# Kernel optimization log

Measured on AMD Instinct MI355X. Metric: run time of the kernel, lower is better.

Reference implementation:

```python
import jax, jax.numpy as jnp
import numpy as np

B, N, M, D, H = 4, 384, 384, 64, 64


def _lin(key, fi, fo):
    kw, kb = jax.random.split(key)
    bound = 1.0 / np.sqrt(fi)
    W = jax.random.uniform(kw, (fi, fo), jnp.float32, -bound, bound)
    b = jax.random.uniform(kb, (fo,), jnp.float32, -bound, bound)
    return W, b


def setup_inputs() -> dict:
    key = jax.random.key(0)
    kX, kY, kp = jax.random.split(key, 3)
    X = jax.random.normal(kX, (B, N, D), jnp.float32)
    Y = jax.random.normal(kY, (B, M, D), jnp.float32)
    ks = jax.random.split(kp, 10)
    inp = {"X": X, "Y": Y}
    # Four pair encoders (e1_xx, e1_xy, e1_yx, e1_yy): Linear(2D,H) -> ReLU -> Linear(H,H)
    for i, tag in enumerate(["xx", "xy", "yx", "yy"]):
        W1, b1 = _lin(ks[2 * i], 2 * D, H)
        W2, b2 = _lin(ks[2 * i + 1], H, H)
        inp[f"W_{tag}1"], inp[f"b_{tag}1"] = W1, b1
        inp[f"W_{tag}2"], inp[f"b_{tag}2"] = W2, b2
    # Decoder: Linear(2H,H) -> ReLU -> Linear(H,1)
    inp["Wd1"], inp["bd1"] = _lin(ks[8], 2 * H, H)
    inp["Wd2"], inp["bd2"] = _lin(ks[9], H, 1)
    return inp


def _pair_branch(A, C, W1, b1, W2, b2):
    """Encode pairs cat(A[b,j], C[b,i]) with MLP, then max over j.

    Instead of materializing the [B,I,J,2D] concat tensor, split the first
    linear layer: cat(a, c) @ W1 == a @ W1[:D] + c @ W1[D:].
    Returns [B, I, H].
    """
    Da = A.shape[-1]
    pa = jnp.einsum('bjd,dh->bjh', A, W1[:Da])   # contribution of A[b, j]
    pc = jnp.einsum('bid,dh->bih', C, W1[Da:])   # contribution of C[b, i]
    pre = pa[:, None, :, :] + pc[:, :, None, :] + b1          # [B, I, J, H]
    h = jnp.einsum('bijh,hk->bijk', jax.nn.relu(pre), W2) + b2  # [B, I, J, H]
    return jnp.max(h, axis=2)                                   # [B, I, H]


def reference(X, Y,
              W_xx1, b_xx1, W_xx2, b_xx2,
              W_xy1, b_xy1, W_xy2, b_xy2,
              W_yx1, b_yx1, W_yx2, b_yx2,
              W_yy1, b_yy1, W_yy2, b_yy2,
              Wd1, bd1, Wd2, bd2):
    # XX[b,i,j] = cat(X[b,j], X[b,i]); YX[b,i,j] = cat(Y[b,j], X[b,i]); etc.
    Z_XX = _pair_branch(X, X, W_xx1, b_xx1, W_xx2, b_xx2)  # [B, N, H]
    Z_YX = _pair_branch(Y, X, W_yx1, b_yx1, W_yx2, b_yx2)  # [B, N, H]
    # Computed in the original forward but never used downstream (dead code):
    Z_YY = _pair_branch(Y, Y, W_yy1, b_yy1, W_yy2, b_yy2)  # noqa: F841
    Z_XY = _pair_branch(X, Y, W_xy1, b_xy1, W_xy2, b_xy2)  # noqa: F841
    # Original source sets Z_Y = Z_XX - Z_YX as well (apparent bug, preserved).
    diff = Z_XX - Z_YX
    Z_X = jnp.sum(diff, axis=1)  # [B, H]
    Z_Y = jnp.sum(diff, axis=1)  # [B, H]
    z = jnp.concatenate([Z_X, Z_Y], axis=-1)        # [B, 2H]
    h = jax.nn.relu(z @ Wd1 + bd1)
    return h @ Wd2 + bd2                             # [B, 1]
```

## Files before the change

### kernel.cpp

```cpp
#include <hip/hip_runtime.h>

#define B_ 4
#define N_ 384
#define D_ 64
#define H_ 64
#define BN_ (B_ * N_)
#define ROW_ (N_ * H_)
#define NTP_ 12
#define LDW_ 68

typedef float f32x4 __attribute__((ext_vector_type(4)));
typedef _Float16 half8 __attribute__((ext_vector_type(8)));
typedef __fp16 fp16x2 __attribute__((ext_vector_type(2)));

union frag_cast { f32x4 f; half8 h; };

__global__ __launch_bounds__(256) void proj_kernel(
    const float* __restrict__ X, const float* __restrict__ Y,
    const float* __restrict__ Wxx1, const float* __restrict__ bxx1,
    const float* __restrict__ Wyx1, const float* __restrict__ byx1,
    const float* __restrict__ W2xx, const float* __restrict__ W2yx,
    float* __restrict__ PAxx, float* __restrict__ PCxx,
    float* __restrict__ PAyx, float* __restrict__ PCyx,
    _Float16* __restrict__ W2F)
{
    if (blockIdx.x >= 384) {
        int t = (blockIdx.x - 384) * 256 + threadIdx.x;
        int br = t >> 10;
        int q  = (t >> 6) & 15;
        int l  = t & 63;
        int nt = q >> 2, kt = (q >> 1) & 1, part = q & 1;
        const float* W2 = br ? W2yx : W2xx;
        int n = nt * 16 + (l & 15);
        int g = l >> 4;
        _Float16* dst = W2F + t * 8;
#pragma unroll
        for (int e = 0; e < 8; ++e) {
            int h = kt * 32 + g * 8 + e;
            float v = W2[h * 64 + n];
            _Float16 hi = (_Float16)v;
            _Float16 lo = (_Float16)(v - (float)hi);
            dst[e] = part ? lo : hi;
        }
        return;
    }

    int blk = blockIdx.x;
    int t = threadIdx.x;
    int which = t >> 6, h = t & 63;

    __shared__ float xr[4][64];
    __shared__ float yr[4][64];
    xr[t >> 6][t & 63] = X[(blk * 4 + (t >> 6)) * 64 + (t & 63)];
    yr[t >> 6][t & 63] = Y[(blk * 4 + (t >> 6)) * 64 + (t & 63)];
    __syncthreads();

    const float (*v)[64] = (which == 2) ? yr : xr;
    const float* W = (which < 2) ? Wxx1 : Wyx1;
    int rowoff = (which & 1) ? 64 : 0;

    float acc[4];
    float binit = 0.f;
    if (which == 1) binit = bxx1[h];
    if (which == 3) binit = byx1[h];
#pragma unroll
    for (int r = 0; r < 4; ++r) acc[r] = binit;

#pragma unroll
    for (int d = 0; d < 64; ++d) {
        float wv = W[(rowoff + d) * 64 + h];
#pragma unroll
        for (int r = 0; r < 4; ++r)
            acc[r] = fmaf(v[r][d], wv, acc[r]);
    }

    float* dst = (which == 0) ? PAxx : (which == 1) ? PCxx
               : (which == 2) ? PAyx : PCyx;
#pragma unroll
    for (int r = 0; r < 4; ++r)
        dst[(blk * 4 + r) * 64 + h] = acc[r];
}

__global__ __launch_bounds__(256, 3) void pair_mfma_kernel(
    const float* __restrict__ PAxx, const float* __restrict__ PCxx,
    const float* __restrict__ PAyx, const float* __restrict__ PCyx,
    const f32x4* __restrict__ W2F,
    float* __restrict__ zxxs, float* __restrict__ zyxs)
{
    int bid = blockIdx.x;
    int blk = (bid & 7) * 96 + (bid >> 3);
    int br = blk / 384;
    int ig = blk % 384;
    int t = threadIdx.x;
    int w = t >> 6, l = t & 63;
    int g = l >> 4, m = l & 15;
    int bi = ig * 4 + w;
    int b  = bi / N_;

    const float* PA = br ? PAyx : PAxx;
    const float* PC = br ? PCyx : PCxx;

    __shared__ float lbuf[2][32 * LDW_];
    __shared__ float zsums[4][64];

    half8 bf[4][2][2];
    const f32x4* Wb = W2F + br * 1024;
#pragma unroll
    for (int q = 0; q < 16; ++q) {
        frag_cast u;
        u.f = Wb[q * 64 + l];
        asm volatile("" : "+v"(u.f));
        bf[q >> 2][(q >> 1) & 1][q & 1] = u.h;
    }

    f32x4 pcq[4];
#pragma unroll
    for (int kt = 0; kt < 2; ++kt) {
        pcq[kt * 2 + 0] = *(const f32x4*)(PC + bi * 64 + kt * 32 + g * 8);
        pcq[kt * 2 + 1] = *(const f32x4*)(PC + bi * 64 + kt * 32 + g * 8 + 4);
    }

    float mm[4] = {-3.0e38f, -3.0e38f, -3.0e38f, -3.0e38f};

    int srow = t >> 4;
    int scg  = t & 15;
    const float* gsrc = PA + b * ROW_ + srow * 64 + scg * 4;
    int soff = srow * LDW_ + scg * 4;

    *(f32x4*)(&lbuf[0][0] + soff) = *(const f32x4*)(gsrc);
    *(f32x4*)(&lbuf[0][0] + soff + 16 * LDW_) = *(const f32x4*)(gsrc + 1024);
    __syncthreads();

    const f32x4 vzero = {0.f, 0.f, 0.f, 0.f};
    int cur = 0;

#pragma unroll 1
    for (int pt = 0; pt < NTP_; ++pt) {
        f32x4 gn0, gn1;
        if (pt + 1 < NTP_) {
            gn0 = *(const f32x4*)(gsrc + (pt + 1) * 2048);
            gn1 = *(const f32x4*)(gsrc + (pt + 1) * 2048 + 1024);
        }

#pragma unroll
        for (int st = 0; st < 2; ++st) {
            const float* lrd = &lbuf[0][0] + cur * (32 * LDW_)
                             + (st * 16 + m) * LDW_ + g * 8;
            f32x4 s0 = *(const f32x4*)(lrd);
            f32x4 s1 = *(const f32x4*)(lrd + 4);
            f32x4 s2 = *(const f32x4*)(lrd + 32);
            f32x4 s3 = *(const f32x4*)(lrd + 36);

            half8 ah[2], al[2];
#pragma unroll
            for (int kt = 0; kt < 2; ++kt) {
                f32x4 xa = (kt ? s2 : s0) + pcq[kt * 2 + 0];
                f32x4 xb = (kt ? s3 : s1) + pcq[kt * 2 + 1];
                xa = __builtin_elementwise_max(xa, vzero);
                xb = __builtin_elementwise_max(xb, vzero);
                fp16x2* ahp = (fp16x2*)&ah[kt];
                fp16x2* alp = (fp16x2*)&al[kt];
#pragma unroll
                for (int p2 = 0; p2 < 2; ++p2) {
                    fp16x2 hpa = __builtin_amdgcn_cvt_pkrtz(xa[p2 * 2], xa[p2 * 2 + 1]);
                    fp16x2 hpb = __builtin_amdgcn_cvt_pkrtz(xb[p2 * 2], xb[p2 * 2 + 1]);
                    ahp[p2]     = hpa;
                    ahp[p2 + 2] = hpb;
                    alp[p2]     = __builtin_amdgcn_cvt_pkrtz(xa[p2 * 2]     - (float)hpa[0],
                                                             xa[p2 * 2 + 1] - (float)hpa[1]);
                    alp[p2 + 2] = __builtin_amdgcn_cvt_pkrtz(xb[p2 * 2]     - (float)hpb[0],
                                                             xb[p2 * 2 + 1] - (float)hpb[1]);
                }
            }

#pragma unroll
            for (int nt = 0; nt < 4; ++nt) {
                f32x4 a = {0.f, 0.f, 0.f, 0.f};
#pragma unroll
                for (int kt = 0; kt < 2; ++kt) {
                    a = __builtin_amdgcn_mfma_f32_16x16x32_f16(ah[kt], bf[nt][kt][0], a, 0, 0, 0);
                    a = __builtin_amdgcn_mfma_f32_16x16x32_f16(ah[kt], bf[nt][kt][1], a, 0, 0, 0);
                    a = __builtin_amdgcn_mfma_f32_16x16x32_f16(al[kt], bf[nt][kt][0], a, 0, 0, 0);
                }
                mm[nt] = fmaxf(mm[nt],
                               fmaxf(fmaxf(a[0], a[1]), fmaxf(a[2], a[3])));
            }
        }

        if (pt + 1 < NTP_) {
            *(f32x4*)(&lbuf[0][0] + (cur ^ 1) * (32 * LDW_) + soff) = gn0;
            *(f32x4*)(&lbuf[0][0] + (cur ^ 1) * (32 * LDW_) + soff + 16 * LDW_) = gn1;
        }
        __syncthreads();
        cur ^= 1;
    }

#pragma unroll
    for (int nt = 0; nt < 4; ++nt) {
        float v = mm[nt];
        v = fmaxf(v, __shfl_xor(v, 16));
        v = fmaxf(v, __shfl_xor(v, 32));
        mm[nt] = v;
    }
    float z = (l < 32) ? ((l < 16) ? mm[0] : mm[1])
                       : ((l < 48) ? mm[2] : mm[3]);

    zsums[w][l] = z;
    __syncthreads();
    if (w == 0) {
        float s = ((zsums[0][l] + zsums[1][l]) + zsums[2][l]) + zsums[3][l];
        (br ? zyxs : zxxs)[ig * 64 + l] = s;
    }
}

__global__ __launch_bounds__(256) void head_kernel(
    const float* __restrict__ zxxs, const float* __restrict__ zyxs,
    const float* __restrict__ b2xx, const float* __restrict__ b2yx,
    const float* __restrict__ Wd1, const float* __restrict__ bd1,
    const float* __restrict__ Wd2, const float* __restrict__ bd2,
    float* __restrict__ out)
{
    int b = blockIdx.x;
    int t = threadIdx.x;
    int ig = t >> 6, h = t & 63;

    __shared__ float sbuf[4][64];
    __shared__ float zx[64];

    float s = 0.f;
    for (int q = ig; q < 96; q += 4) {
        int idx = (b * 96 + q) * 64 + h;
        s += zxxs[idx] - zyxs[idx];
    }
    sbuf[ig][h] = s;
    __syncthreads();
    if (t < 64)
        zx[t] = sbuf[0][t] + sbuf[1][t] + sbuf[2][t] + sbuf[3][t]
              + (float)N_ * (b2xx[t] - b2yx[t]);
    __syncthreads();

    if (t < 64) {
        float acc = bd1[t];
#pragma unroll
        for (int d = 0; d < 64; ++d)
            acc = fmaf(zx[d], Wd1[d * 64 + t] + Wd1[(64 + d) * 64 + t], acc);
        float h1 = fmaxf(acc, 0.f);
        float r = h1 * Wd2[t];
#pragma unroll
        for (int off = 32; off; off >>= 1) r += __shfl_down(r, off);
        if (t == 0) out[b] = r + bd2[0];
    }
}

extern "C" void kernel_launch(void* const* d_in, const int* in_sizes, int n_in,
                              void* d_out, int out_size, void* d_ws, size_t ws_size,
                              hipStream_t stream) {
    const float* X    = (const float*)d_in[0];
    const float* Y    = (const float*)d_in[1];
    const float* Wxx1 = (const float*)d_in[2];
    const float* bxx1 = (const float*)d_in[3];
    const float* W2xx = (const float*)d_in[4];
    const float* b2xx = (const float*)d_in[5];
    const float* Wyx1 = (const float*)d_in[10];
    const float* byx1 = (const float*)d_in[11];
    const float* W2yx = (const float*)d_in[12];
    const float* b2yx = (const float*)d_in[13];
    const float* Wd1  = (const float*)d_in[18];
    const float* bd1  = (const float*)d_in[19];
    const float* Wd2  = (const float*)d_in[20];
    const float* bd2  = (const float*)d_in[21];

    float* ws   = (float*)d_ws;
    float* PAxx = ws;
    float* PCxx = ws + 1 * (BN_ * H_);
    float* PAyx = ws + 2 * (BN_ * H_);
    float* PCyx = ws + 3 * (BN_ * H_);
    float* zxxs = ws + 4 * (BN_ * H_);
    float* zyxs = ws + 4 * (BN_ * H_) + 384 * 64;
    _Float16* W2F = (_Float16*)(ws + 5 * (BN_ * H_));

    proj_kernel<<<384 + 8, 256, 0, stream>>>(X, Y, Wxx1, bxx1, Wyx1, byx1,
                                             W2xx, W2yx,
                                             PAxx, PCxx, PAyx, PCyx, W2F);
    pair_mfma_kernel<<<768, 256, 0, stream>>>(PAxx, PCxx, PAyx, PCyx,
                                              (const f32x4*)W2F, zxxs, zyxs);
    head_kernel<<<B_, 256, 0, stream>>>(zxxs, zyxs, b2xx, b2yx,
                                        Wd1, bd1, Wd2, bd2, (float*)d_out);
}
```

Baseline: 47.40 us.

## Switch pair MLP matmul from 16x16x32 to 32x32x16 MFMA tiles

Changes the second-layer pair matmul to use 32x32x16 f16 MFMA instructions with 16-element accumulators, covering 32 j-rows per wave in one pass instead of two 16-row subtiles. The W2 fragment preparation in the projection kernel and the B-fragment layout are rearranged to match the new operand layout. The max reduction over j shrinks to one cross-lane shuffle. The intent is to cut instruction count, LDS reads and shuffle overhead per tile, at the cost of larger accumulator register pressure, which may hurt occupancy at three waves per SIMD.

```diff
diff --git a/kernel.cpp b/kernel.cpp
--- a/kernel.cpp
+++ b/kernel.cpp
@@ -10,6 +10,7 @@
 #define LDW_ 68
 
 typedef float f32x4 __attribute__((ext_vector_type(4)));
+typedef float f32x16 __attribute__((ext_vector_type(16)));
 typedef _Float16 half8 __attribute__((ext_vector_type(8)));
 typedef __fp16 fp16x2 __attribute__((ext_vector_type(2)));
 
@@ -29,14 +30,14 @@
         int br = t >> 10;
         int q  = (t >> 6) & 15;
         int l  = t & 63;
-        int nt = q >> 2, kt = (q >> 1) & 1, part = q & 1;
+        int hc = q >> 3, ks = (q >> 1) & 3, part = q & 1;
         const float* W2 = br ? W2yx : W2xx;
-        int n = nt * 16 + (l & 15);
-        int g = l >> 4;
+        int n  = hc * 32 + (l & 31);
+        int g2 = l >> 5;
         _Float16* dst = W2F + t * 8;
 #pragma unroll
         for (int e = 0; e < 8; ++e) {
-            int h = kt * 32 + g * 8 + e;
+            int h = ks * 16 + g2 * 8 + e;
             float v = W2[h * 64 + n];
             _Float16 hi = (_Float16)v;
             _Float16 lo = (_Float16)(v - (float)hi);
@@ -93,7 +94,7 @@
     int ig = blk % 384;
     int t = threadIdx.x;
     int w = t >> 6, l = t & 63;
-    int g = l >> 4, m = l & 15;
+    int g2 = l >> 5, m32 = l & 31;
     int bi = ig * 4 + w;
     int b  = bi / N_;
 
@@ -103,24 +104,24 @@
     __shared__ float lbuf[2][32 * LDW_];
     __shared__ float zsums[4][64];
 
-    half8 bf[4][2][2];
+    half8 bf[2][4][2];
     const f32x4* Wb = W2F + br * 1024;
 #pragma unroll
     for (int q = 0; q < 16; ++q) {
         frag_cast u;
         u.f = Wb[q * 64 + l];
         asm volatile("" : "+v"(u.f));
-        bf[q >> 2][(q >> 1) & 1][q & 1] = u.h;
-    }
-
-    f32x4 pcq[4];
-#pragma unroll
-    for (int kt = 0; kt < 2; ++kt) {
-        pcq[kt * 2 + 0] = *(const f32x4*)(PC + bi * 64 + kt * 32 + g * 8);
-        pcq[kt * 2 + 1] = *(const f32x4*)(PC + bi * 64 + kt * 32 + g * 8 + 4);
-    }
-
-    float mm[4] = {-3.0e38f, -3.0e38f, -3.0e38f, -3.0e38f};
+        bf[q >> 3][(q >> 1) & 3][q & 1] = u.h;
+    }
+
+    f32x4 pcq[8];
+#pragma unroll
+    for (int ks = 0; ks < 4; ++ks) {
+        pcq[ks * 2 + 0] = *(const f32x4*)(PC + bi * 64 + ks * 16 + g2 * 8);
+        pcq[ks * 2 + 1] = *(const f32x4*)(PC + bi * 64 + ks * 16 + g2 * 8 + 4);
+    }
+
+    float mm[2] = {-3.0e38f, -3.0e38f};
 
     int srow = t >> 4;
     int scg  = t & 15;
@@ -142,49 +143,56 @@
             gn1 = *(const f32x4*)(gsrc + (pt + 1) * 2048 + 1024);
         }
 
-#pragma unroll
-        for (int st = 0; st < 2; ++st) {
-            const float* lrd = &lbuf[0][0] + cur * (32 * LDW_)
-                             + (st * 16 + m) * LDW_ + g * 8;
-            f32x4 s0 = *(const f32x4*)(lrd);
-            f32x4 s1 = *(const f32x4*)(lrd + 4);
-            f32x4 s2 = *(const f32x4*)(lrd + 32);
-            f32x4 s3 = *(const f32x4*)(lrd + 36);
-
-            half8 ah[2], al[2];
-#pragma unroll
-            for (int kt = 0; kt < 2; ++kt) {
-                f32x4 xa = (kt ? s2 : s0) + pcq[kt * 2 + 0];
-                f32x4 xb = (kt ? s3 : s1) + pcq[kt * 2 + 1];
-                xa = __builtin_elementwise_max(xa, vzero);
-                xb = __builtin_elementwise_max(xb, vzero);
-                fp16x2* ahp = (fp16x2*)&ah[kt];
-                fp16x2* alp = (fp16x2*)&al[kt];
-#pragma unroll
-                for (int p2 = 0; p2 < 2; ++p2) {
-                    fp16x2 hpa = __builtin_amdgcn_cvt_pkrtz(xa[p2 * 2], xa[p2 * 2 + 1]);
-                    fp16x2 hpb = __builtin_amdgcn_cvt_pkrtz(xb[p2 * 2], xb[p2 * 2 + 1]);
-                    ahp[p2]     = hpa;
-                    ahp[p2 + 2] = hpb;
-                    alp[p2]     = __builtin_amdgcn_cvt_pkrtz(xa[p2 * 2]     - (float)hpa[0],
-                                                             xa[p2 * 2 + 1] - (float)hpa[1]);
-                    alp[p2 + 2] = __builtin_amdgcn_cvt_pkrtz(xb[p2 * 2]     - (float)hpb[0],
-                                                             xb[p2 * 2 + 1] - (float)hpb[1]);
-                }
+        f32x16 acc0 = {0.f,0.f,0.f,0.f,0.f,0.f,0.f,0.f,
+                       0.f,0.f,0.f,0.f,0.f,0.f,0.f,0.f};
+        f32x16 acc1 = {0.f,0.f,0.f,0.f,0.f,0.f,0.f,0.f,
+                       0.f,0.f,0.f,0.f,0.f,0.f,0.f,0.f};
+
+        const float* rowbase = &lbuf[0][0] + cur * (32 * LDW_) + m32 * LDW_;
+
+#pragma unroll
+        for (int ks = 0; ks < 4; ++ks) {
+            f32x4 s0 = *(const f32x4*)(rowbase + ks * 16 + g2 * 8);
+            f32x4 s1 = *(const f32x4*)(rowbase + ks * 16 + g2 * 8 + 4);
+
+            f32x4 xa = s0 + pcq[ks * 2 + 0];
+            f32x4 xb = s1 + pcq[ks * 2 + 1];
+            xa = __builtin_elementwise_max(xa, vzero);
+            xb = __builtin_elementwise_max(xb, vzero);
+            half8 ah, al;
+            fp16x2* ahp = (fp16x2*)&ah;
+            fp16x2* alp = (fp16x2*)&al;
+#pragma unroll
+            for (int p2 = 0; p2 < 2; ++p2) {
+                fp16x2 hpa = __builtin_amdgcn_cvt_pkrtz(xa[p2 * 2], xa[p2 * 2 + 1]);
+                fp16x2 hpb = __builtin_amdgcn_cvt_pkrtz(xb[p2 * 2], xb[p2 * 2 + 1]);
+                ahp[p2]     = hpa;
+                ahp[p2 + 2] = hpb;
+                alp[p2]     = __builtin_amdgcn_cvt_pkrtz(xa[p2 * 2]     - (float)hpa[0],
+                                                         xa[p2 * 2 + 1] - (float)hpa[1]);
+                alp[p2 + 2] = __builtin_amdgcn_cvt_pkrtz(xb[p2 * 2]     - (float)hpb[0],
+                                                         xb[p2 * 2 + 1] - (float)hpb[1]);
             }
 
-#pragma unroll
-            for (int nt = 0; nt < 4; ++nt) {
-                f32x4 a = {0.f, 0.f, 0.f, 0.f};
-#pragma unroll
-                for (int kt = 0; kt < 2; ++kt) {
-                    a = __builtin_amdgcn_mfma_f32_16x16x32_f16(ah[kt], bf[nt][kt][0], a, 0, 0, 0);
-                    a = __builtin_amdgcn_mfma_f32_16x16x32_f16(ah[kt], bf[nt][kt][1], a, 0, 0, 0);
-                    a = __builtin_amdgcn_mfma_f32_16x16x32_f16(al[kt], bf[nt][kt][0], a, 0, 0, 0);
-                }
-                mm[nt] = fmaxf(mm[nt],
-                               fmaxf(fmaxf(a[0], a[1]), fmaxf(a[2], a[3])));
-            }
+            acc0 = __builtin_amdgcn_mfma_f32_32x32x16_f16(ah, bf[0][ks][0], acc0, 0, 0, 0);
+            acc1 = __builtin_amdgcn_mfma_f32_32x32x16_f16(ah, bf[1][ks][0], acc1, 0, 0, 0);
+            acc0 = __builtin_amdgcn_mfma_f32_32x32x16_f16(al, bf[0][ks][0], acc0, 0, 0, 0);
+            acc1 = __builtin_amdgcn_mfma_f32_32x32x16_f16(al, bf[1][ks][0], acc1, 0, 0, 0);
+            acc0 = __builtin_amdgcn_mfma_f32_32x32x16_f16(ah, bf[0][ks][1], acc0, 0, 0, 0);
+            acc1 = __builtin_amdgcn_mfma_f32_32x32x16_f16(ah, bf[1][ks][1], acc1, 0, 0, 0);
+        }
+
+        {
+            float a0 = fmaxf(fmaxf(acc0[0], acc0[1]), fmaxf(acc0[2], acc0[3]));
+            float a1 = fmaxf(fmaxf(acc0[4], acc0[5]), fmaxf(acc0[6], acc0[7]));
+            float a2 = fmaxf(fmaxf(acc0[8], acc0[9]), fmaxf(acc0[10], acc0[11]));
+            float a3 = fmaxf(fmaxf(acc0[12], acc0[13]), fmaxf(acc0[14], acc0[15]));
+            mm[0] = fmaxf(mm[0], fmaxf(fmaxf(a0, a1), fmaxf(a2, a3)));
+            float c0 = fmaxf(fmaxf(acc1[0], acc1[1]), fmaxf(acc1[2], acc1[3]));
+            float c1 = fmaxf(fmaxf(acc1[4], acc1[5]), fmaxf(acc1[6], acc1[7]));
+            float c2 = fmaxf(fmaxf(acc1[8], acc1[9]), fmaxf(acc1[10], acc1[11]));
+            float c3 = fmaxf(fmaxf(acc1[12], acc1[13]), fmaxf(acc1[14], acc1[15]));
+            mm[1] = fmaxf(mm[1], fmaxf(fmaxf(c0, c1), fmaxf(c2, c3)));
         }
 
         if (pt + 1 < NTP_) {
@@ -195,15 +203,9 @@
         cur ^= 1;
     }
 
-#pragma unroll
-    for (int nt = 0; nt < 4; ++nt) {
-        float v = mm[nt];
-        v = fmaxf(v, __shfl_xor(v, 16));
-        v = fmaxf(v, __shfl_xor(v, 32));
-        mm[nt] = v;
-    }
-    float z = (l < 32) ? ((l < 16) ? mm[0] : mm[1])
-                       : ((l < 48) ? mm[2] : mm[3]);
+    float v0 = fmaxf(mm[0], __shfl_xor(mm[0], 32));
+    float v1 = fmaxf(mm[1], __shfl_xor(mm[1], 32));
+    float z = (l < 32) ? v0 : v1;
 
     zsums[w][l] = z;
     __syncthreads();
```

Result: slower. 48.73 us (+2.8%).
